# Kernel optimization log

Measured on AMD Instinct MI355X. Metric: run time of the kernel, lower is better.

## Reference

```python
import jax, jax.numpy as jnp
import numpy as np

B, TD, TE, H = 8, 128, 256, 512


def setup_inputs() -> dict:
    key = jax.random.key(0)
    k1, k2, k3, k4, k5, k6 = jax.random.split(key, 6)
    enc = jax.random.normal(k1, (B, TE, H), dtype=jnp.float32)
    dec = jax.random.normal(k2, (B, TD, H), dtype=jnp.float32)
    mask = jax.random.randint(k3, (B, TE), 0, 2).astype(jnp.bool_)
    # glorot-ish scale for weights
    W1 = jax.random.normal(k4, (H, H), dtype=jnp.float32) * (1.0 / np.sqrt(H))
    W2 = jax.random.normal(k5, (H, H), dtype=jnp.float32) * (1.0 / np.sqrt(H))
    V = jax.random.normal(k6, (H, 1), dtype=jnp.float32) * (1.0 / np.sqrt(H))
    return {"encoder_outputs": enc, "decoder_outputs": dec,
            "encoder_mask": mask, "W1": W1, "W2": W2, "V": V}


def reference(encoder_outputs, decoder_outputs, encoder_mask, W1, W2, V):
    # Bahdanau additive attention.
    # enc: [B, Te, H], dec: [B, Td, H], mask: [B, Te]
    ew = jnp.einsum('bsh,hk->bsk', encoder_outputs, W1)   # [B, Te, H]
    dw = jnp.einsum('bth,hk->btk', decoder_outputs, W2)   # [B, Td, H]
    # broadcast add -> [B, Td, Te, H] (the large intermediate)
    s = jnp.tanh(ew[:, None, :, :] + dw[:, :, None, :])
    score = jnp.einsum('btsh,h->bts', s, V[:, 0])          # [B, Td, Te]
    m = encoder_mask.astype(jnp.float32)                   # [B, Te]
    score = score + (1.0 - m)[:, None, :] * (-1e9)
    attention_weights = jax.nn.softmax(score, axis=2)      # [B, Td, Te]
    context_vector = jnp.einsum('bts,bsh->bth', attention_weights, encoder_outputs)
    return context_vector, attention_weights
```

## Files before the change

kernel.cpp:

```cpp
#include <hip/hip_runtime.h>
#include <hip/hip_bf16.h>
#include <math.h>

constexpr int kB  = 8;
constexpr int kTD = 128;
constexpr int kTE = 256;
constexpr int kH  = 512;

constexpr float kTwoLog2e = 2.8853900817779268f;
constexpr float kLog2e    = 1.4426950408889634f;

constexpr int TM = 4;
constexpr int GEMM_BLOCKS = 384;

typedef __attribute__((ext_vector_type(8)))  short short8;
typedef __attribute__((ext_vector_type(16))) float f32x16;

__device__ __forceinline__ unsigned short f2bf(float x) {
    unsigned int u = __float_as_uint(x);
    return (unsigned short)((u + 0x7fffu + ((u >> 16) & 1u)) >> 16);
}
__device__ __forceinline__ float bf2f(unsigned short h) {
    return __uint_as_float(((unsigned int)h) << 16);
}

__global__ __launch_bounds__(256)
void prep_kernel(const float* __restrict__ enc, const float* __restrict__ dec,
                 const float* __restrict__ W1, const float* __restrict__ W2,
                 const void* __restrict__ mask_raw,
                 float* __restrict__ ewt, float* __restrict__ dwc,
                 float* __restrict__ mask_f) {
    const int bx = blockIdx.x;
    const int tid = threadIdx.x;

    if (bx == GEMM_BLOCKS) {
        const unsigned int* w = (const unsigned int*)mask_raw;
        unsigned int gt1 = 0, flt = 0;
        for (int i = tid; i < 512; i += 256) {
            unsigned int v = w[i];
            if (v == 0x3f800000u) flt = 1;
            else if (v > 1u) gt1 = 1;
        }
        __shared__ unsigned int s_gt1, s_flt;
        if (tid == 0) { s_gt1 = 0u; s_flt = 0u; }
        __syncthreads();
        if (gt1) atomicOr(&s_gt1, 1u);
        if (flt) atomicOr(&s_flt, 1u);
        __syncthreads();
        const int mode = s_flt ? 2 : (s_gt1 ? 1 : 0);
        for (int i = tid; i < kB * kTE; i += 256) {
            float val;
            if (mode == 2)      val = ((const float*)mask_raw)[i];
            else if (mode == 1) val = (float)(((const unsigned char*)mask_raw)[i]);
            else                val = (float)(((const int*)mask_raw)[i]);
            mask_f[i] = val;
        }
        return;
    }

    const int mt = bx >> 3;
    const int nt = bx & 7;
    const bool is_enc = (mt < 32);
    const int m0 = mt * 64;
    const int n0 = nt * 64;
    const float* Abase = is_enc ? (enc + (size_t)m0 * kH)
                                : (dec + (size_t)(m0 - 2048) * kH);
    const float* W = is_enc ? W1 : W2;

    __shared__ __align__(16) unsigned short Ahi[64][40], Alo[64][40];
    __shared__ __align__(16) unsigned short Bhi[64][40], Blo[64][40];
    __shared__ float Ws[32][68];

    const int lane = tid & 63;
    const int wv   = tid >> 6;
    const int wr   = wv >> 1, wc = wv & 1;
    const int col  = lane & 31, hi5 = lane >> 5;

    const int ar  = tid >> 2;
    const int akc = (tid & 3) * 8;
    const int wkr = tid >> 3;
    const int wnc = (tid & 7) * 8;
    const int pn  = tid & 63;
    const int pkc = (tid >> 6) * 8;

    f32x16 acc = {};

    float4 a0p = *(const float4*)&Abase[(size_t)ar * kH + akc];
    float4 a1p = *(const float4*)&Abase[(size_t)ar * kH + akc + 4];
    float4 w0p = *(const float4*)&W[(size_t)wkr * kH + n0 + wnc];
    float4 w1p = *(const float4*)&W[(size_t)wkr * kH + n0 + wnc + 4];

    for (int step = 0; step < 16; ++step) {
        *(float4*)&Ws[wkr][wnc]     = w0p;
        *(float4*)&Ws[wkr][wnc + 4] = w1p;
        {
            uint4 H, L;
            float f[8] = {a0p.x, a0p.y, a0p.z, a0p.w, a1p.x, a1p.y, a1p.z, a1p.w};
            unsigned short hs[8], ls[8];
            #pragma unroll
            for (int j = 0; j < 8; ++j) {
                hs[j] = f2bf(f[j]);
                ls[j] = f2bf(f[j] - bf2f(hs[j]));
            }
            H.x = hs[0] | (hs[1] << 16); H.y = hs[2] | (hs[3] << 16);
            H.z = hs[4] | (hs[5] << 16); H.w = hs[6] | (hs[7] << 16);
            L.x = ls[0] | (ls[1] << 16); L.y = ls[2] | (ls[3] << 16);
            L.z = ls[4] | (ls[5] << 16); L.w = ls[6] | (ls[7] << 16);
            *(uint4*)&Ahi[ar][akc] = H;
            *(uint4*)&Alo[ar][akc] = L;
        }
        __syncthreads();

        {
            uint4 H, L;
            unsigned short hs[8], ls[8];
            #pragma unroll
            for (int j = 0; j < 8; ++j) {
                float x = Ws[pkc + j][pn];
                hs[j] = f2bf(x);
                ls[j] = f2bf(x - bf2f(hs[j]));
            }
            H.x = hs[0] | (hs[1] << 16); H.y = hs[2] | (hs[3] << 16);
            H.z = hs[4] | (hs[5] << 16); H.w = hs[6] | (hs[7] << 16);
            L.x = ls[0] | (ls[1] << 16); L.y = ls[2] | (ls[3] << 16);
            L.z = ls[4] | (ls[5] << 16); L.w = ls[6] | (ls[7] << 16);
            *(uint4*)&Bhi[pn][pkc] = H;
            *(uint4*)&Blo[pn][pkc] = L;
        }

        if (step < 15) {
            const int k1 = (step + 1) * 32;
            a0p = *(const float4*)&Abase[(size_t)ar * kH + k1 + akc];
            a1p = *(const float4*)&Abase[(size_t)ar * kH + k1 + akc + 4];
            w0p = *(const float4*)&W[(size_t)(k1 + wkr) * kH + n0 + wnc];
            w1p = *(const float4*)&W[(size_t)(k1 + wkr) * kH + n0 + wnc + 4];
        }
        __syncthreads();

        #pragma unroll
        for (int kc = 0; kc < 32; kc += 16) {
            const int ka = kc + hi5 * 8;
            short8 ah = *(const short8*)&Ahi[wr * 32 + col][ka];
            short8 al = *(const short8*)&Alo[wr * 32 + col][ka];
            short8 bh = *(const short8*)&Bhi[wc * 32 + col][ka];
            short8 bl = *(const short8*)&Blo[wc * 32 + col][ka];
            acc = __builtin_amdgcn_mfma_f32_32x32x16_bf16(ah, bh, acc, 0, 0, 0);
            acc = __builtin_amdgcn_mfma_f32_32x32x16_bf16(ah, bl, acc, 0, 0, 0);
            acc = __builtin_amdgcn_mfma_f32_32x32x16_bf16(al, bh, acc, 0, 0, 0);
        }
        __syncthreads();
    }

    const int h = n0 + wc * 32 + col;
    if (is_enc) {
        #pragma unroll
        for (int reg = 0; reg < 16; ++reg) {
            const int row = (reg & 3) + 8 * (reg >> 2) + 4 * hi5;
            const int gm = m0 + wr * 32 + row;
            const int bb = gm >> 8, sE = gm & 255;
            float val = __builtin_amdgcn_exp2f(acc[reg] * kTwoLog2e);
            ewt[(((size_t)bb * 128 + (h >> 2)) * 256 + sE) * 4 + (h & 3)] = val;
        }
    } else {
        #pragma unroll
        for (int reg = 0; reg < 16; ++reg) {
            const int row = (reg & 3) + 8 * (reg >> 2) + 4 * hi5;
            const int dm = (m0 - 2048) + wr * 32 + row;
            float val = __builtin_amdgcn_exp2f(acc[reg] * kTwoLog2e);
            dwc[(size_t)dm * kH + h] = val;
        }
    }
}

__global__ __launch_bounds__(1024)
void fused_attn_kernel(const float* __restrict__ ewt, const float* __restrict__ dwc,
                       const float* __restrict__ enc, const float* __restrict__ V,
                       const float* __restrict__ mask_f,
                       float* __restrict__ ctx_out, float* __restrict__ attn_out) {
    const int bid = blockIdx.x;
    const int b   = bid & 7;
    const int t0  = (bid >> 3) * TM;
    const int tid = threadIdx.x;
    const int s   = tid & 255;
    const int hq  = tid >> 8;
    const int hqu = __builtin_amdgcn_readfirstlane(hq);

    __shared__ union {
        float  part[3 * TM * kTE];
        float4 pctx[4][TM][128];
    } u;
    __shared__ float4 wgt4[kTE];
    __shared__ float red_mx[4][TM], red_sm[4][TM];

    const float4* E4 = (const float4*)ewt + ((size_t)(b * 128 + hqu * 32) * 256 + s);
    const float4* Pb = (const float4*)(dwc + (size_t)(b * kTD + t0) * kH) + hqu * 32;
    const float4* V4 = (const float4*)V + hqu * 32;

    float a0 = 0.0f, a1 = 0.0f, a2 = 0.0f, a3 = 0.0f;
    #pragma unroll 4
    for (int g = 0; g < 32; ++g) {
        float4 e  = E4[(size_t)g * 256];
        float4 vv = V4[g];
        {   float4 q = Pb[g];
            float A_ = fmaf(e.x, q.x, 1.0f), B_ = fmaf(e.y, q.y, 1.0f);
            float C_ = fmaf(e.z, q.z, 1.0f), D_ = fmaf(e.w, q.w, 1.0f);
            float t1 = fmaf(vv.y, A_, vv.x * B_);
            float t2 = fmaf(vv.w, C_, vv.z * D_);
            float AB = A_ * B_, CD = C_ * D_;
            float num = fmaf(t2, AB, t1 * CD);
            a0 = fmaf(num, __builtin_amdgcn_rcpf(AB * CD), a0); }
        {   float4 q = Pb[128 + g];
            float A_ = fmaf(e.x, q.x, 1.0f), B_ = fmaf(e.y, q.y, 1.0f);
            float C_ = fmaf(e.z, q.z, 1.0f), D_ = fmaf(e.w, q.w, 1.0f);
            float t1 = fmaf(vv.y, A_, vv.x * B_);
            float t2 = fmaf(vv.w, C_, vv.z * D_);
            float AB = A_ * B_, CD = C_ * D_;
            float num = fmaf(t2, AB, t1 * CD);
            a1 = fmaf(num, __builtin_amdgcn_rcpf(AB * CD), a1); }
        {   float4 q = Pb[256 + g];
            float A_ = fmaf(e.x, q.x, 1.0f), B_ = fmaf(e.y, q.y, 1.0f);
            float C_ = fmaf(e.z, q.z, 1.0f), D_ = fmaf(e.w, q.w, 1.0f);
            float t1 = fmaf(vv.y, A_, vv.x * B_);
            float t2 = fmaf(vv.w, C_, vv.z * D_);
            float AB = A_ * B_, CD = C_ * D_;
            float num = fmaf(t2, AB, t1 * CD);
            a2 = fmaf(num, __builtin_amdgcn_rcpf(AB * CD), a2); }
        {   float4 q = Pb[384 + g];
            float A_ = fmaf(e.x, q.x, 1.0f), B_ = fmaf(e.y, q.y, 1.0f);
            float C_ = fmaf(e.z, q.z, 1.0f), D_ = fmaf(e.w, q.w, 1.0f);
            float t1 = fmaf(vv.y, A_, vv.x * B_);
            float t2 = fmaf(vv.w, C_, vv.z * D_);
            float AB = A_ * B_, CD = C_ * D_;
            float num = fmaf(t2, AB, t1 * CD);
            a3 = fmaf(num, __builtin_amdgcn_rcpf(AB * CD), a3); }
    }

    if (hq > 0) {
        float* pp = &u.part[(hq - 1) * TM * kTE];
        pp[0 * kTE + s] = a0; pp[1 * kTE + s] = a1;
        pp[2 * kTE + s] = a2; pp[3 * kTE + s] = a3;
    }
    __syncthreads();

    const bool active = (hq == 0);
    const int wvq = s >> 6;
    float sc0, sc1, sc2, sc3;
    if (active) {
        const float* P = u.part;
        const float pen = (1.0f - mask_f[b * kTE + s]) * -1e9f;
        sc0 = -2.0f * ((a0 + P[0 * TM * kTE + 0 * kTE + s]) +
                       (P[1 * TM * kTE + 0 * kTE + s] + P[2 * TM * kTE + 0 * kTE + s])) + pen;
        sc1 = -2.0f * ((a1 + P[0 * TM * kTE + 1 * kTE + s]) +
                       (P[1 * TM * kTE + 1 * kTE + s] + P[2 * TM * kTE + 1 * kTE + s])) + pen;
        sc2 = -2.0f * ((a2 + P[0 * TM * kTE + 2 * kTE + s]) +
                       (P[1 * TM * kTE + 2 * kTE + s] + P[2 * TM * kTE + 2 * kTE + s])) + pen;
        sc3 = -2.0f * ((a3 + P[0 * TM * kTE + 3 * kTE + s]) +
                       (P[1 * TM * kTE + 3 * kTE + s] + P[2 * TM * kTE + 3 * kTE + s])) + pen;
        float m0 = sc0, m1 = sc1, m2 = sc2, m3 = sc3;
        #pragma unroll
        for (int off = 1; off < 64; off <<= 1) {
            m0 = fmaxf(m0, __shfl_xor(m0, off));
            m1 = fmaxf(m1, __shfl_xor(m1, off));
            m2 = fmaxf(m2, __shfl_xor(m2, off));
            m3 = fmaxf(m3, __shfl_xor(m3, off));
        }
        if ((s & 63) == 0) {
            red_mx[wvq][0] = m0; red_mx[wvq][1] = m1;
            red_mx[wvq][2] = m2; red_mx[wvq][3] = m3;
        }
    }
    __syncthreads();

    float p0, p1, p2, p3;
    if (active) {
        float m0 = fmaxf(fmaxf(red_mx[0][0], red_mx[1][0]), fmaxf(red_mx[2][0], red_mx[3][0]));
        float m1 = fmaxf(fmaxf(red_mx[0][1], red_mx[1][1]), fmaxf(red_mx[2][1], red_mx[3][1]));
        float m2 = fmaxf(fmaxf(red_mx[0][2], red_mx[1][2]), fmaxf(red_mx[2][2], red_mx[3][2]));
        float m3 = fmaxf(fmaxf(red_mx[0][3], red_mx[1][3]), fmaxf(red_mx[2][3], red_mx[3][3]));
        p0 = __builtin_amdgcn_exp2f((sc0 - m0) * kLog2e);
        p1 = __builtin_amdgcn_exp2f((sc1 - m1) * kLog2e);
        p2 = __builtin_amdgcn_exp2f((sc2 - m2) * kLog2e);
        p3 = __builtin_amdgcn_exp2f((sc3 - m3) * kLog2e);
        float s0 = p0, s1 = p1, s2 = p2, s3 = p3;
        #pragma unroll
        for (int off = 1; off < 64; off <<= 1) {
            s0 += __shfl_xor(s0, off);
            s1 += __shfl_xor(s1, off);
            s2 += __shfl_xor(s2, off);
            s3 += __shfl_xor(s3, off);
        }
        if ((s & 63) == 0) {
            red_sm[wvq][0] = s0; red_sm[wvq][1] = s1;
            red_sm[wvq][2] = s2; red_sm[wvq][3] = s3;
        }
    }
    __syncthreads();

    if (active) {
        float s0 = (red_sm[0][0] + red_sm[1][0]) + (red_sm[2][0] + red_sm[3][0]);
        float s1 = (red_sm[0][1] + red_sm[1][1]) + (red_sm[2][1] + red_sm[3][1]);
        float s2 = (red_sm[0][2] + red_sm[1][2]) + (red_sm[2][2] + red_sm[3][2]);
        float s3 = (red_sm[0][3] + red_sm[1][3]) + (red_sm[2][3] + red_sm[3][3]);
        float4 w;
        w.x = p0 * __builtin_amdgcn_rcpf(s0);
        w.y = p1 * __builtin_amdgcn_rcpf(s1);
        w.z = p2 * __builtin_amdgcn_rcpf(s2);
        w.w = p3 * __builtin_amdgcn_rcpf(s3);
        wgt4[s] = w;
        float* ao = attn_out + (size_t)(b * kTD + t0) * kTE + s;
        ao[0]       = w.x;
        ao[kTE]     = w.y;
        ao[2 * kTE] = w.z;
        ao[3 * kTE] = w.w;
    }
    __syncthreads();

    const int th4 = tid & 127;
    const int sq  = tid >> 7;
    const float4* enc4 = (const float4*)(enc + (size_t)b * kTE * kH);
    float4 c[TM];
    #pragma unroll
    for (int t = 0; t < TM; ++t) c[t] = float4{0.f, 0.f, 0.f, 0.f};
    #pragma unroll 4
    for (int i = 0; i < 32; ++i) {
        const int ss = sq * 32 + i;
        float4 e = enc4[(size_t)ss * 128 + th4];
        float4 w = wgt4[ss];
        c[0].x = fmaf(w.x, e.x, c[0].x); c[0].y = fmaf(w.x, e.y, c[0].y);
        c[0].z = fmaf(w.x, e.z, c[0].z); c[0].w = fmaf(w.x, e.w, c[0].w);
        c[1].x = fmaf(w.y, e.x, c[1].x); c[1].y = fmaf(w.y, e.y, c[1].y);
        c[1].z = fmaf(w.y, e.z, c[1].z); c[1].w = fmaf(w.y, e.w, c[1].w);
        c[2].x = fmaf(w.z, e.x, c[2].x); c[2].y = fmaf(w.z, e.y, c[2].y);
        c[2].z = fmaf(w.z, e.z, c[2].z); c[2].w = fmaf(w.z, e.w, c[2].w);
        c[3].x = fmaf(w.w, e.x, c[3].x); c[3].y = fmaf(w.w, e.y, c[3].y);
        c[3].z = fmaf(w.w, e.z, c[3].z); c[3].w = fmaf(w.w, e.w, c[3].w);
    }
    if (sq >= 4) {
        #pragma unroll
        for (int t = 0; t < TM; ++t) u.pctx[sq - 4][t][th4] = c[t];
    }
    __syncthreads();
    if (sq < 4) {
        #pragma unroll
        for (int t = 0; t < TM; ++t) {
            float4 p = u.pctx[sq][t][th4];
            c[t].x += p.x; c[t].y += p.y; c[t].z += p.z; c[t].w += p.w;
        }
    }
    __syncthreads();
    if (sq >= 1 && sq < 4) {
        #pragma unroll
        for (int t = 0; t < TM; ++t) u.pctx[sq - 1][t][th4] = c[t];
    }
    __syncthreads();
    if (sq == 0) {
        #pragma unroll
        for (int t = 0; t < TM; ++t) {
            float4 q0v = u.pctx[0][t][th4];
            float4 q1v = u.pctx[1][t][th4];
            float4 q2v = u.pctx[2][t][th4];
            c[t].x += (q0v.x + q1v.x) + q2v.x;
            c[t].y += (q0v.y + q1v.y) + q2v.y;
            c[t].z += (q0v.z + q1v.z) + q2v.z;
            c[t].w += (q0v.w + q1v.w) + q2v.w;
            *(float4*)&ctx_out[(size_t)(b * kTD + t0 + t) * kH + th4 * 4] = c[t];
        }
    }
}

extern "C" void kernel_launch(void* const* d_in, const int* in_sizes, int n_in,
                              void* d_out, int out_size, void* d_ws, size_t ws_size,
                              hipStream_t stream) {
    const float* enc  = (const float*)d_in[0];
    const float* dec  = (const float*)d_in[1];
    const void*  mask = d_in[2];
    const float* W1   = (const float*)d_in[3];
    const float* W2   = (const float*)d_in[4];
    const float* V    = (const float*)d_in[5];

    float* ctx_out  = (float*)d_out;
    float* attn_out = (float*)d_out + kB * kTD * kH;

    char* ws = (char*)d_ws;
    float* mask_f = (float*)ws;
    float* ewt    = (float*)(ws + 8192);
    float* dwc    = (float*)(ws + 8192 + (size_t)kB * kTE * kH * 4);

    hipLaunchKernelGGL(prep_kernel, dim3(GEMM_BLOCKS + 1), dim3(256), 0, stream,
                       enc, dec, W1, W2, mask, ewt, dwc, mask_f);
    hipLaunchKernelGGL(fused_attn_kernel, dim3(kB * kTD / TM), dim3(1024), 0, stream,
                       ewt, dwc, enc, V, mask_f, ctx_out, attn_out);
}
```

Before: 43.87 us.

## Share converted weight tile across two M-tiles per 512-thread prep block

The projection GEMM blocks grow to 512 threads, and each block computes two adjacent 64-row M-tiles against the same 64-column weight tile. The weight tile is loaded and split into bf16 hi/lo parts once and then used by both halves. This halves the weight global loads and the conversion work per output tile. In exchange the grid shrinks from 384 to 192 GEMM blocks, fewer than the number of CUs, and the larger blocks may reduce occupancy.

```diff
diff --git a/kernel.cpp b/kernel.cpp
--- a/kernel.cpp
+++ b/kernel.cpp
@@ -11,7 +11,7 @@
 constexpr float kLog2e    = 1.4426950408889634f;
 
 constexpr int TM = 4;
-constexpr int GEMM_BLOCKS = 384;
+constexpr int GEMM_BLOCKS = 192;
 
 typedef __attribute__((ext_vector_type(8)))  short short8;
 typedef __attribute__((ext_vector_type(16))) float f32x16;
@@ -24,7 +24,7 @@
     return __uint_as_float(((unsigned int)h) << 16);
 }
 
-__global__ __launch_bounds__(256)
+__global__ __launch_bounds__(512)
 void prep_kernel(const float* __restrict__ enc, const float* __restrict__ dec,
                  const float* __restrict__ W1, const float* __restrict__ W2,
                  const void* __restrict__ mask_raw,
@@ -36,8 +36,8 @@
     if (bx == GEMM_BLOCKS) {
         const unsigned int* w = (const unsigned int*)mask_raw;
         unsigned int gt1 = 0, flt = 0;
-        for (int i = tid; i < 512; i += 256) {
-            unsigned int v = w[i];
+        if (tid < 512) {
+            unsigned int v = w[tid];
             if (v == 0x3f800000u) flt = 1;
             else if (v > 1u) gt1 = 1;
         }
@@ -48,7 +48,7 @@
         if (flt) atomicOr(&s_flt, 1u);
         __syncthreads();
         const int mode = s_flt ? 2 : (s_gt1 ? 1 : 0);
-        for (int i = tid; i < kB * kTE; i += 256) {
+        for (int i = tid; i < kB * kTE; i += 512) {
             float val;
             if (mode == 2)      val = ((const float*)mask_raw)[i];
             else if (mode == 1) val = (float)(((const unsigned char*)mask_raw)[i]);
@@ -58,41 +58,44 @@
         return;
     }
 
-    const int mt = bx >> 3;
+    const int pt = bx >> 3;
     const int nt = bx & 7;
-    const bool is_enc = (mt < 32);
-    const int m0 = mt * 64;
+    const bool is_enc = (pt < 16);
+    const int mt0 = is_enc ? (pt * 2) : (32 + (pt - 16) * 2);
     const int n0 = nt * 64;
+
+    const int g   = tid >> 8;
+    const int lid = tid & 255;
+    const int mt  = mt0 + g;
+    const int m0  = mt * 64;
     const float* Abase = is_enc ? (enc + (size_t)m0 * kH)
                                 : (dec + (size_t)(m0 - 2048) * kH);
     const float* W = is_enc ? W1 : W2;
 
-    __shared__ __align__(16) unsigned short Ahi[64][40], Alo[64][40];
+    __shared__ __align__(16) unsigned short Ahi[2][64][40], Alo[2][64][40];
     __shared__ __align__(16) unsigned short Bhi[64][40], Blo[64][40];
     __shared__ float Ws[32][68];
 
     const int lane = tid & 63;
-    const int wv   = tid >> 6;
-    const int wr   = wv >> 1, wc = wv & 1;
+    const int gw   = (tid >> 6) & 3;
+    const int wr   = gw >> 1, wc = gw & 1;
     const int col  = lane & 31, hi5 = lane >> 5;
 
-    const int ar  = tid >> 2;
-    const int akc = (tid & 3) * 8;
-    const int wkr = tid >> 3;
-    const int wnc = (tid & 7) * 8;
+    const int ar  = lid >> 2;
+    const int akc = (lid & 3) * 8;
+    const int wkr = tid >> 4;
+    const int wnc = (tid & 15) * 4;
     const int pn  = tid & 63;
-    const int pkc = (tid >> 6) * 8;
+    const int pkc = ((tid >> 6) & 3) * 8;
 
     f32x16 acc = {};
 
     float4 a0p = *(const float4*)&Abase[(size_t)ar * kH + akc];
     float4 a1p = *(const float4*)&Abase[(size_t)ar * kH + akc + 4];
     float4 w0p = *(const float4*)&W[(size_t)wkr * kH + n0 + wnc];
-    float4 w1p = *(const float4*)&W[(size_t)wkr * kH + n0 + wnc + 4];
 
     for (int step = 0; step < 16; ++step) {
-        *(float4*)&Ws[wkr][wnc]     = w0p;
-        *(float4*)&Ws[wkr][wnc + 4] = w1p;
+        *(float4*)&Ws[wkr][wnc] = w0p;
         {
             uint4 H, L;
             float f[8] = {a0p.x, a0p.y, a0p.z, a0p.w, a1p.x, a1p.y, a1p.z, a1p.w};
@@ -106,12 +109,12 @@
             H.z = hs[4] | (hs[5] << 16); H.w = hs[6] | (hs[7] << 16);
             L.x = ls[0] | (ls[1] << 16); L.y = ls[2] | (ls[3] << 16);
             L.z = ls[4] | (ls[5] << 16); L.w = ls[6] | (ls[7] << 16);
-            *(uint4*)&Ahi[ar][akc] = H;
-            *(uint4*)&Alo[ar][akc] = L;
-        }
-        __syncthreads();
-
-        {
+            *(uint4*)&Ahi[g][ar][akc] = H;
+            *(uint4*)&Alo[g][ar][akc] = L;
+        }
+        __syncthreads();
+
+        if (tid < 256) {
             uint4 H, L;
             unsigned short hs[8], ls[8];
             #pragma unroll
@@ -133,15 +136,14 @@
             a0p = *(const float4*)&Abase[(size_t)ar * kH + k1 + akc];
             a1p = *(const float4*)&Abase[(size_t)ar * kH + k1 + akc + 4];
             w0p = *(const float4*)&W[(size_t)(k1 + wkr) * kH + n0 + wnc];
-            w1p = *(const float4*)&W[(size_t)(k1 + wkr) * kH + n0 + wnc + 4];
         }
         __syncthreads();
 
         #pragma unroll
         for (int kc = 0; kc < 32; kc += 16) {
             const int ka = kc + hi5 * 8;
-            short8 ah = *(const short8*)&Ahi[wr * 32 + col][ka];
-            short8 al = *(const short8*)&Alo[wr * 32 + col][ka];
+            short8 ah = *(const short8*)&Ahi[g][wr * 32 + col][ka];
+            short8 al = *(const short8*)&Alo[g][wr * 32 + col][ka];
             short8 bh = *(const short8*)&Bhi[wc * 32 + col][ka];
             short8 bl = *(const short8*)&Blo[wc * 32 + col][ka];
             acc = __builtin_amdgcn_mfma_f32_32x32x16_bf16(ah, bh, acc, 0, 0, 0);
@@ -386,7 +388,7 @@
     float* ewt    = (float*)(ws + 8192);
     float* dwc    = (float*)(ws + 8192 + (size_t)kB * kTE * kH * 4);
 
-    hipLaunchKernelGGL(prep_kernel, dim3(GEMM_BLOCKS + 1), dim3(256), 0, stream,
+    hipLaunchKernelGGL(prep_kernel, dim3(GEMM_BLOCKS + 1), dim3(512), 0, stream,
                        enc, dec, W1, W2, mask, ewt, dwc, mask_f);
     hipLaunchKernelGGL(fused_attn_kernel, dim3(kB * kTD / TM), dim3(1024), 0, stream,
                        ewt, dwc, enc, V, mask_f, ctx_out, attn_out);
```

After: 42.25 us, median of 2. -3.7%, faster.
